# Kernel tuning notes

Measured on AMD Instinct MI355X. Metric: run time of the kernel, lower is better.

## Reference

```python
import jax, jax.numpy as jnp
import numpy as np

N = 100000
E = 1600000
DIN = 128
H = 4
C1 = 32   # hidden_dim per head, layer 1
C2 = 64   # output_dim, layer 2 (heads=1)
NEG_SLOPE = 0.2


def setup_inputs() -> dict:
    key = jax.random.key(0)
    ks = jax.random.split(key, 16)
    x = jax.random.normal(ks[0], (N, DIN), dtype=jnp.float32)
    src = jax.random.randint(ks[1], (E,), 0, N, dtype=jnp.int64)
    off = jax.random.randint(ks[2], (E,), 1, N, dtype=jnp.int64)
    dst = (src + off) % N  # guaranteed no self loops
    edge_index = jnp.stack([src, dst], axis=0)
    edge_weight = jax.random.uniform(ks[3], (E,), dtype=jnp.float32)
    g = 0.1
    # layer 1 params (heads=4, concat)
    W1 = jax.random.normal(ks[4], (DIN, H * C1), dtype=jnp.float32) * g
    att_src1 = jax.random.normal(ks[5], (H, C1), dtype=jnp.float32) * g
    att_dst1 = jax.random.normal(ks[6], (H, C1), dtype=jnp.float32) * g
    att_edge1 = jax.random.normal(ks[7], (H, C1), dtype=jnp.float32) * g
    We1 = jax.random.normal(ks[8], (1, H * C1), dtype=jnp.float32) * g
    b1 = jnp.zeros((H * C1,), dtype=jnp.float32)
    # layer 2 params (heads=1, no concat)
    W2 = jax.random.normal(ks[9], (H * C1, C2), dtype=jnp.float32) * g
    att_src2 = jax.random.normal(ks[10], (1, C2), dtype=jnp.float32) * g
    att_dst2 = jax.random.normal(ks[11], (1, C2), dtype=jnp.float32) * g
    att_edge2 = jax.random.normal(ks[12], (1, C2), dtype=jnp.float32) * g
    We2 = jax.random.normal(ks[13], (1, C2), dtype=jnp.float32) * g
    b2 = jnp.zeros((C2,), dtype=jnp.float32)
    return dict(x=x, edge_index=edge_index, edge_weight=edge_weight,
                W1=W1, att_src1=att_src1, att_dst1=att_dst1, att_edge1=att_edge1, We1=We1, b1=b1,
                W2=W2, att_src2=att_src2, att_dst2=att_dst2, att_edge2=att_edge2, We2=We2, b2=b2)


def gat_conv(x, src, dst, ew, W, a_src, a_dst, a_edge, We, b, heads, out_ch, concat):
    n = x.shape[0]
    xs = (x @ W).reshape(n, heads, out_ch)                 # [N,H,C]
    alpha_src = (xs * a_src[None]).sum(-1)                 # [N,H]
    alpha_dst = (xs * a_dst[None]).sum(-1)                 # [N,H]
    e = (ew[:, None] @ We).reshape(-1, heads, out_ch)      # [E,H,C]
    alpha_edge = (e * a_edge[None]).sum(-1)                # [E,H]
    alpha = alpha_src[src] + alpha_dst[dst] + alpha_edge   # [E,H]
    alpha = jax.nn.leaky_relu(alpha, NEG_SLOPE)
    # segment softmax over destination nodes (every node has a self loop)
    m = jax.ops.segment_max(alpha, dst, num_segments=n)
    ex = jnp.exp(alpha - m[dst])
    s = jax.ops.segment_sum(ex, dst, num_segments=n)
    att = ex / (s[dst] + 1e-16)                            # [E,H]
    out = jax.ops.segment_sum(xs[src] * att[:, :, None], dst, num_segments=n)  # [N,H,C]
    out = out.reshape(n, heads * out_ch) if concat else out.mean(axis=1)
    return out + b


def reference(x, edge_index, edge_weight,
              W1, att_src1, att_dst1, att_edge1, We1, b1,
              W2, att_src2, att_dst2, att_edge2, We2, b2):
    n = x.shape[0]
    src, dst = edge_index[0], edge_index[1]
    # add self loops with fill_value='mean' for edge weights (PyG default)
    si = jnp.arange(n, dtype=src.dtype)
    src2 = jnp.concatenate([src, si])
    dst2 = jnp.concatenate([dst, si])
    ew2 = jnp.concatenate([edge_weight, jnp.full((n,), edge_weight.mean(), dtype=edge_weight.dtype)])
    h = gat_conv(x, src2, dst2, ew2, W1, att_src1, att_dst1, att_edge1, We1, b1, H, C1, True)
    h = jax.nn.elu(h)
    # dropout is identity in eval mode
    out = gat_conv(h, src2, dst2, ew2, W2, att_src2, att_dst2, att_edge2, We2, b2, 1, C2, False)
    return out
```

## Files before the change

### kernel.cpp

```cpp
#include <hip/hip_runtime.h>
#include <hip/hip_fp16.h>
#include <math.h>

#define NN 100000
#define NE 1600000
#define DIN 128
#define NH 4
#define C1 32
#define C2 64
#define NEG 0.2f

#define SCAN_CHUNK 1024
#define NBLK ((NN + SCAN_CHUNK - 1) / SCAN_CHUNK)

#define NBUCK 8
#define BUCKN (NN / NBUCK)
#define CAPB 300000
#define BIN_CHUNK 4096
#define NBINBLK ((NE + BIN_CHUNK - 1) / BIN_CHUNK)

typedef __attribute__((ext_vector_type(8))) short bf16x8;
typedef __attribute__((ext_vector_type(4))) float f32x4;

__device__ __forceinline__ unsigned bf16rtn(float f) {
    unsigned b = __float_as_uint(f);
    return (b + 0x7FFFu + ((b >> 16) & 1u)) >> 16;
}
__device__ __forceinline__ unsigned pack2bf(float lo, float hi) {
    return bf16rtn(lo) | (bf16rtn(hi) << 16);
}
__device__ __forceinline__ unsigned pack2h(float lo, float hi) {
    unsigned a = __half_as_ushort(__float2half(lo));
    unsigned b = __half_as_ushort(__float2half(hi));
    return a | (b << 16);
}
__device__ __forceinline__ float h2f_bits(unsigned short u) {
    return __half2float(__ushort_as_half(u));
}

__global__ void k_setup(const float* __restrict__ We1, const float* __restrict__ ae1,
                        const float* __restrict__ We2, const float* __restrict__ ae2,
                        float* __restrict__ params) {
    __shared__ float sm[128];
    int t = threadIdx.x;
    sm[t] = We1[t] * ae1[t];
    __syncthreads();
    if (t < 4) {
        float s = 0.f;
        for (int c = 0; c < 32; c++) s += sm[t * 32 + c];
        params[2 + t] = s;
    }
    __syncthreads();
    if (t < 64) sm[t] = We2[t] * ae2[t];
    __syncthreads();
    if (t == 0) {
        float s = 0.f;
        for (int c = 0; c < 64; c++) s += sm[c];
        params[6] = s;
        params[1] = params[0] / (float)NE;
    }
}

__global__ void k_wprep(const float* __restrict__ W1, const float* __restrict__ W2,
                        uint4* __restrict__ wfrag1, uint4* __restrict__ wfrag2) {
    int t = blockIdx.x * 256 + threadIdx.x;
    if (t < 2048) {
        int f = t >> 6, l = t & 63;
        int n = f & 7, kc = f >> 3;
        int col = n * 16 + (l & 15);
        int kb = kc * 32 + (l >> 4) * 8;
        const float* p = W1 + (size_t)kb * 128 + col;
        uint4 pk;
        pk.x = pack2bf(p[0], p[128]);
        pk.y = pack2bf(p[256], p[384]);
        pk.z = pack2bf(p[512], p[640]);
        pk.w = pack2bf(p[768], p[896]);
        wfrag1[t] = pk;
    } else if (t < 3072) {
        int s = t - 2048;
        int f = s >> 6, l = s & 63;
        int n = f & 3, kc = f >> 2;
        int col = n * 16 + (l & 15);
        int kb = kc * 32 + (l >> 4) * 8;
        const float* p = W2 + (size_t)kb * 64 + col;
        uint4 pk;
        pk.x = pack2bf(p[0], p[64]);
        pk.y = pack2bf(p[128], p[192]);
        pk.z = pack2bf(p[256], p[320]);
        pk.w = pack2bf(p[384], p[448]);
        wfrag2[s] = pk;
    }
}

__global__ void k_binA(const int* __restrict__ srcI, const int* __restrict__ dstI,
                       const float* __restrict__ ew, int* __restrict__ bcur,
                       int* __restrict__ bdst, int2* __restrict__ bse,
                       float* __restrict__ params) {
    __shared__ int hcnt[NBUCK], hbase[NBUCK], hoff[NBUCK];
    int t = threadIdx.x;
    int e0 = blockIdx.x * BIN_CHUNK;
    if (t < NBUCK) hcnt[t] = 0;
    __syncthreads();
    for (int i = t; i < BIN_CHUNK; i += 256) {
        int e = e0 + i;
        if (e < NE) atomicAdd(&hcnt[dstI[e] / BUCKN], 1);
    }
    __syncthreads();
    if (t < NBUCK) { hbase[t] = atomicAdd(&bcur[t], hcnt[t]); hoff[t] = 0; }
    __syncthreads();
    float locw = 0.f;
    for (int i = t; i < BIN_CHUNK; i += 256) {
        int e = e0 + i;
        if (e < NE) {
            int d = dstI[e];
            float w = ew[e];
            locw += w;
            int b = d / BUCKN;
            int p = b * CAPB + hbase[b] + atomicAdd(&hoff[b], 1);
            bdst[p] = d;
            bse[p] = make_int2(srcI[e], __float_as_int(w));
        }
    }
    for (int o = 32; o > 0; o >>= 1) locw += __shfl_down(locw, o, 64);
    if ((t & 63) == 0) atomicAdd(&params[0], locw);
}

__global__ void k_histB(const int* __restrict__ bdst, const int* __restrict__ bcur,
                        int* __restrict__ deg) {
    int b = blockIdx.x & (NBUCK - 1);
    int slice = blockIdx.x >> 3;
    int cnt = bcur[b];
    int lo = b * CAPB;
    int per = (cnt + 255) / 256;
    int s0 = lo + slice * per;
    int s1 = min(s0 + per, lo + cnt);
    for (int i = s0 + threadIdx.x; i < s1; i += 256)
        atomicAdd(&deg[bdst[i]], 1);
}

__global__ void k_scanA(const int* __restrict__ deg, int* __restrict__ bsum) {
    __shared__ int ws[4];
    int b = blockIdx.x;
    int base = b * SCAN_CHUNK;
    int t = threadIdx.x;
    int s = 0;
    for (int i = t; i < SCAN_CHUNK; i += 256) {
        int idx = base + i;
        if (idx < NN) s += deg[idx];
    }
    for (int o = 32; o > 0; o >>= 1) s += __shfl_down(s, o, 64);
    int lane = t & 63, wid = t >> 6;
    if (lane == 0) ws[wid] = s;
    __syncthreads();
    if (t == 0) bsum[b] = ws[0] + ws[1] + ws[2] + ws[3];
}

__global__ void k_scanB(const int* __restrict__ bsum, int* __restrict__ bpre,
                        int* __restrict__ rowptr) {
    __shared__ int wtot[2];
    int t = threadIdx.x;
    int lane = t & 63, wid = t >> 6;
    int v = (t < NBLK) ? bsum[t] : 0;
    int inc = v;
    for (int o = 1; o < 64; o <<= 1) { int u = __shfl_up(inc, o, 64); if (lane >= o) inc += u; }
    if (lane == 63) wtot[wid] = inc;
    __syncthreads();
    if (wid == 1) inc += wtot[0];
    if (t < NBLK) bpre[t] = inc - v;
    if (t == NBLK - 1) rowptr[NN] = inc;
}

__global__ void k_scanC(const int* __restrict__ deg, const int* __restrict__ bpre,
                        int* __restrict__ rowptr, int* __restrict__ cursor) {
    __shared__ int wtot[4];
    int b = blockIdx.x;
    int t = threadIdx.x;
    int lane = t & 63, wid = t >> 6;
    int idx0 = b * SCAN_CHUNK + t * 4;
    int d[4];
    int s = 0;
    #pragma unroll
    for (int j = 0; j < 4; j++) {
        int idx = idx0 + j;
        d[j] = (idx < NN) ? deg[idx] : 0;
        s += d[j];
    }
    int inc = s;
    for (int o = 1; o < 64; o <<= 1) { int u = __shfl_up(inc, o, 64); if (lane >= o) inc += u; }
    if (lane == 63) wtot[wid] = inc;
    __syncthreads();
    int add = bpre[b];
    for (int w = 0; w < wid; w++) add += wtot[w];
    int excl = inc - s + add;
    #pragma unroll
    for (int j = 0; j < 4; j++) {
        int idx = idx0 + j;
        if (idx < NN) { rowptr[idx] = excl; cursor[idx] = excl; }
        excl += d[j];
    }
}

__global__ void k_binB(const int* __restrict__ bdst, const int2* __restrict__ bse,
                       const int* __restrict__ bcur, int* __restrict__ cursor,
                       const float* __restrict__ as1, const float* __restrict__ ad1,
                       const float* __restrict__ params, int4* __restrict__ edge4) {
    int b = blockIdx.x & (NBUCK - 1);
    int slice = blockIdx.x >> 3;
    int cnt = bcur[b];
    int lo = b * CAPB;
    int per = (cnt + 255) / 256;
    int s0 = lo + slice * per;
    int s1 = min(s0 + per, lo + cnt);
    float ce0 = params[2], ce1 = params[3], ce2 = params[4], ce3 = params[5];
    for (int i = s0 + threadIdx.x; i < s1; i += 256) {
        int d = bdst[i];
        int2 se = bse[i];
        float w = __int_as_float(se.y);
        float4 a1 = *(const float4*)(as1 + (size_t)se.x * 4);
        float4 d1 = *(const float4*)(ad1 + (size_t)d * 4);
        float q0 = a1.x + d1.x + w * ce0; q0 = q0 > 0.f ? q0 : NEG * q0;
        float q1 = a1.y + d1.y + w * ce1; q1 = q1 > 0.f ? q1 : NEG * q1;
        float q2 = a1.z + d1.z + w * ce2; q2 = q2 > 0.f ? q2 : NEG * q2;
        float q3 = a1.w + d1.w + w * ce3; q3 = q3 > 0.f ? q3 : NEG * q3;
        q0 = __expf(q0); q1 = __expf(q1); q2 = __expf(q2); q3 = __expf(q3);
        int idx = atomicAdd(&cursor[d], 1);
        edge4[idx] = make_int4(se.x, se.y, (int)pack2h(q0, q1), (int)pack2h(q2, q3));
    }
}


__global__ void __launch_bounds__(256, 4)
k_gemm1(const float* __restrict__ x, const uint4* __restrict__ wfrag1,
        const float* __restrict__ asv, const float* __restrict__ adv,
        unsigned* __restrict__ xs1b, float* __restrict__ as1, float* __restrict__ ad1) {
    __shared__ uint4 smem[2112];
    int t = threadIdx.x;
    for (int i = t; i < 2048; i += 256) smem[i] = wfrag1[i];
    __syncthreads();
    int wid = t >> 6, lane = t & 63;
    int r0 = blockIdx.x * 64 + wid * 16;
    int rowA = r0 + (lane & 15);
    int kb = (lane >> 4) * 8;
    bf16x8 afr[4];
    if (rowA < NN) {
        const float* xr = x + (size_t)rowA * 128 + kb;
        #pragma unroll
        for (int kc = 0; kc < 4; kc++) {
            float4 u0 = *(const float4*)(xr + kc * 32);
            float4 u1 = *(const float4*)(xr + kc * 32 + 4);
            uint4 p = make_uint4(pack2bf(u0.x, u0.y), pack2bf(u0.z, u0.w),
                                 pack2bf(u1.x, u1.y), pack2bf(u1.z, u1.w));
            afr[kc] = *(bf16x8*)&p;
        }
    } else {
        uint4 z = make_uint4(0u, 0u, 0u, 0u);
        #pragma unroll
        for (int kc = 0; kc < 4; kc++) afr[kc] = *(bf16x8*)&z;
    }
    f32x4 acc[8];
    #pragma unroll
    for (int n = 0; n < 8; n++) acc[n] = (f32x4){0.f, 0.f, 0.f, 0.f};
    #pragma unroll
    for (int kc = 0; kc < 4; kc++) {
        #pragma unroll
        for (int n = 0; n < 8; n++) {
            uint4 bw = smem[(kc * 8 + n) * 64 + lane];
            acc[n] = __builtin_amdgcn_mfma_f32_16x16x32_bf16(afr[kc], *(bf16x8*)&bw, acc[n], 0, 0, 0);
        }
    }
    __syncthreads();
    float* ef = (float*)smem + wid * 2112;
    #pragma unroll
    for (int n = 0; n < 8; n++) {
        #pragma unroll
        for (int r = 0; r < 4; r++) {
            int rw = (lane >> 4) * 4 + r;
            int col = n * 16 + (lane & 15);
            ef[rw * 132 + (col >> 5) * 33 + (col & 31)] = acc[n][r];
        }
    }
    __syncthreads();
    int rw = lane >> 2, head = lane & 3;
    int row = r0 + rw;
    if (row < NN) {
        const float* rb = ef + rw * 132 + head * 33;
        const float* av = asv + head * 32;
        const float* dv = adv + head * 32;
        unsigned* orow = xs1b + (size_t)row * 64 + head * 16;
        float ps = 0.f, pd = 0.f;
        #pragma unroll
        for (int j = 0; j < 4; j++) {
            float v[8];
            #pragma unroll
            for (int e = 0; e < 8; e++) {
                v[e] = rb[8 * j + e];
                ps += v[e] * av[8 * j + e];
                pd += v[e] * dv[8 * j + e];
            }
            uint4 pk = make_uint4(pack2bf(v[0], v[1]), pack2bf(v[2], v[3]),
                                  pack2bf(v[4], v[5]), pack2bf(v[6], v[7]));
            *(uint4*)(orow + 4 * j) = pk;
        }
        as1[row * 4 + head] = ps;
        ad1[row * 4 + head] = pd;
    }
}


__global__ void k_agg1(const unsigned* __restrict__ xs1b, const float* __restrict__ as1,
                       const float* __restrict__ ad1, const int* __restrict__ rowptr,
                       const int4* __restrict__ edge4,
                       const float* __restrict__ params, const float* __restrict__ b1,
                       unsigned* __restrict__ h1b) {
    int wid = threadIdx.x >> 6, lane = threadIdx.x & 63;
    int n = blockIdx.x * 4 + wid;
    if (n >= NN) return;
    int h = lane >> 4;
    float meanw = params[1];
    float aself = as1[n * 4 + h] + ad1[n * 4 + h] + meanw * params[2 + h];
    aself = aself > 0.f ? aself : NEG * aself;
    float qs = __expf(aself);
    unsigned us = xs1b[(size_t)n * 64 + lane];
    float s  = qs;
    float ax = qs * __uint_as_float(us << 16);
    float ay = qs * __uint_as_float(us & 0xFFFF0000u);
    int lo = rowptr[n], hi = rowptr[n + 1];
    int hlo = h < 2, hodd = h & 1;
    int i = lo;
    for (; i + 8 <= hi; i += 8) {
        int cj[8]; float qj[8]; unsigned vv[8];
        #pragma unroll
        for (int u = 0; u < 8; u++) {
            int4 er = edge4[i + u];
            cj[u] = er.x;
            unsigned qw = hlo ? (unsigned)er.z : (unsigned)er.w;
            qw = hodd ? (qw >> 16) : (qw & 0xFFFFu);
            qj[u] = h2f_bits((unsigned short)qw);
        }
        #pragma unroll
        for (int u = 0; u < 8; u++) vv[u] = xs1b[(size_t)cj[u] * 64 + lane];
        #pragma unroll
        for (int u = 0; u < 8; u++) {
            s += qj[u];
            ax += qj[u] * __uint_as_float(vv[u] << 16);
            ay += qj[u] * __uint_as_float(vv[u] & 0xFFFF0000u);
        }
    }
    for (; i < hi; i++) {
        int4 er = edge4[i];
        unsigned qw = hlo ? (unsigned)er.z : (unsigned)er.w;
        qw = hodd ? (qw >> 16) : (qw & 0xFFFFu);
        float qj = h2f_bits((unsigned short)qw);
        unsigned u = xs1b[(size_t)er.x * 64 + lane];
        s += qj;
        ax += qj * __uint_as_float(u << 16);
        ay += qj * __uint_as_float(u & 0xFFFF0000u);
    }
    float inv = 1.0f / (s + 1e-16f);
    float o0 = ax * inv + b1[2 * lane];
    float o1 = ay * inv + b1[2 * lane + 1];
    o0 = o0 > 0.f ? o0 : (__expf(o0) - 1.0f);
    o1 = o1 > 0.f ? o1 : (__expf(o1) - 1.0f);
    h1b[(size_t)n * 64 + lane] = pack2bf(o0, o1);
}


__global__ void __launch_bounds__(256, 6)
k_gemm2(const unsigned* __restrict__ h1b, const uint4* __restrict__ wfrag2,
        const float* __restrict__ asv, const float* __restrict__ adv,
        unsigned* __restrict__ xs2b, float* __restrict__ as2, float* __restrict__ ad2) {
    __shared__ uint4 smem[1056];
    int t = threadIdx.x;
    for (int i = t; i < 1024; i += 256) smem[i] = wfrag2[i];
    __syncthreads();
    int wid = t >> 6, lane = t & 63;
    int r0 = blockIdx.x * 64 + wid * 16;
    int rowA = r0 + (lane & 15);
    bf16x8 afr[4];
    if (rowA < NN) {
        const uint4* hr = (const uint4*)(h1b + (size_t)rowA * 64);
        #pragma unroll
        for (int kc = 0; kc < 4; kc++) {
            uint4 p = hr[kc * 4 + (lane >> 4)];
            afr[kc] = *(bf16x8*)&p;
        }
    } else {
        uint4 z = make_uint4(0u, 0u, 0u, 0u);
        #pragma unroll
        for (int kc = 0; kc < 4; kc++) afr[kc] = *(bf16x8*)&z;
    }
    f32x4 acc[4];
    #pragma unroll
    for (int n = 0; n < 4; n++) acc[n] = (f32x4){0.f, 0.f, 0.f, 0.f};
    #pragma unroll
    for (int kc = 0; kc < 4; kc++) {
        #pragma unroll
        for (int n = 0; n < 4; n++) {
            uint4 bw = smem[(kc * 4 + n) * 64 + lane];
            acc[n] = __builtin_amdgcn_mfma_f32_16x16x32_bf16(afr[kc], *(bf16x8*)&bw, acc[n], 0, 0, 0);
        }
    }
    __syncthreads();
    float* ef = (float*)smem + wid * 1056;
    #pragma unroll
    for (int n = 0; n < 4; n++) {
        #pragma unroll
        for (int r = 0; r < 4; r++) {
            int rw = (lane >> 4) * 4 + r;
            int col = n * 16 + (lane & 15);
            ef[rw * 66 + (col >> 5) * 33 + (col & 31)] = acc[n][r];
        }
    }
    __syncthreads();
    int rw = lane >> 2, q = lane & 3;
    int row = r0 + rw;
    const float* rb = ef + rw * 66 + (q >> 1) * 33 + (q & 1) * 16;
    const float* av = asv + q * 16;
    const float* dv = adv + q * 16;
    float ps = 0.f, pd = 0.f;
    unsigned pk[4];
    #pragma unroll
    for (int j = 0; j < 2; j++) {
        float v[8];
        #pragma unroll
        for (int e = 0; e < 8; e++) {
            v[e] = rb[8 * j + e];
            ps += v[e] * av[8 * j + e];
            pd += v[e] * dv[8 * j + e];
        }
        pk[0] = pack2bf(v[0], v[1]); pk[1] = pack2bf(v[2], v[3]);
        pk[2] = pack2bf(v[4], v[5]); pk[3] = pack2bf(v[6], v[7]);
        if (row < NN)
            *(uint4*)(xs2b + (size_t)row * 32 + q * 8 + 4 * j) = make_uint4(pk[0], pk[1], pk[2], pk[3]);
    }
    ps += __shfl_xor(ps, 1, 64); ps += __shfl_xor(ps, 2, 64);
    pd += __shfl_xor(pd, 1, 64); pd += __shfl_xor(pd, 2, 64);
    if (q == 0 && row < NN) { as2[row] = ps; ad2[row] = pd; }
}

__global__ void k_alpha2(int4* __restrict__ edge4, const float* __restrict__ as2,
                         const float* __restrict__ ad2, const int* __restrict__ rowptr,
                         const float* __restrict__ params) {
    int wid = threadIdx.x >> 6, lane = threadIdx.x & 63;
    int n = blockIdx.x * 4 + wid;
    if (n >= NN) return;
    float ce = params[6];
    float adn = ad2[n];
    int lo = rowptr[n], hi = rowptr[n + 1];
    for (int i = lo + lane; i < hi; i += 64) {
        int2 er = *(const int2*)&edge4[i];
        float a = as2[er.x] + adn + __int_as_float(er.y) * ce;
        a = a > 0.f ? a : NEG * a;
        ((int*)&edge4[i])[1] = __float_as_int(__expf(a));
    }
}


__global__ void k_agg2(const unsigned short* __restrict__ xs2h, const float* __restrict__ as2,
                       const float* __restrict__ ad2, const int* __restrict__ rowptr,
                       const int4* __restrict__ edge4,
                       const float* __restrict__ params, const float* __restrict__ b2,
                       float* __restrict__ out) {
    int wid = threadIdx.x >> 6, lane = threadIdx.x & 63;
    int n = blockIdx.x * 4 + wid;
    if (n >= NN) return;
    float ce = params[6];
    float meanw = params[1];
    float adn = ad2[n];
    float aself = as2[n] + adn + meanw * ce;
    aself = aself > 0.f ? aself : NEG * aself;
    float qs = __expf(aself);
    float s = qs;
    float ac = qs * __uint_as_float(((unsigned)xs2h[(size_t)n * 64 + lane]) << 16);
    int lo = rowptr[n], hi = rowptr[n + 1];
    int i = lo;
    for (; i + 8 <= hi; i += 8) {
        int cj[8]; float qj[8]; unsigned short vv[8];
        #pragma unroll
        for (int u = 0; u < 8; u++) {
            int2 er = *(const int2*)&edge4[i + u];
            cj[u] = er.x;
            qj[u] = __int_as_float(er.y);
        }
        #pragma unroll
        for (int u = 0; u < 8; u++) vv[u] = xs2h[(size_t)cj[u] * 64 + lane];
        #pragma unroll
        for (int u = 0; u < 8; u++) {
            s += qj[u];
            ac += qj[u] * __uint_as_float(((unsigned)vv[u]) << 16);
        }
    }
    for (; i < hi; i++) {
        int2 er = *(const int2*)&edge4[i];
        float qj = __int_as_float(er.y);
        float v = __uint_as_float(((unsigned)xs2h[(size_t)er.x * 64 + lane]) << 16);
        s += qj;
        ac += qj * v;
    }
    out[(size_t)n * 64 + lane] = ac / (s + 1e-16f) + b2[lane];
}

extern "C" void kernel_launch(void* const* d_in, const int* in_sizes, int n_in,
                              void* d_out, int out_size, void* d_ws, size_t ws_size,
                              hipStream_t stream) {
    const float* x    = (const float*)d_in[0];
    const int*   ei   = (const int*)d_in[1];
    const float* ew   = (const float*)d_in[2];
    const float* W1   = (const float*)d_in[3];
    const float* as1v = (const float*)d_in[4];
    const float* ad1v = (const float*)d_in[5];
    const float* ae1v = (const float*)d_in[6];
    const float* We1  = (const float*)d_in[7];
    const float* b1   = (const float*)d_in[8];
    const float* W2   = (const float*)d_in[9];
    const float* as2v = (const float*)d_in[10];
    const float* ad2v = (const float*)d_in[11];
    const float* ae2v = (const float*)d_in[12];
    const float* We2  = (const float*)d_in[13];
    const float* b2   = (const float*)d_in[14];
    const int* srcI = ei;
    const int* dstI = ei + NE;

    float* wsf = (float*)d_ws;
    size_t off = 0;
    auto alloc = [&](size_t nelts) { float* p = wsf + off; off += (nelts + 63) & ~(size_t)63; return p; };
    float*    params = alloc(64);
    int*      deg    = (int*)alloc(NN);
    int*      bcur   = (int*)alloc(64);
    int*      rowptr = (int*)alloc(NN + 1);
    int*      cursor = (int*)alloc(NN);
    int*      bsum   = (int*)alloc(NBLK);
    int*      bpre   = (int*)alloc(NBLK);
    uint4*    wfrag1 = (uint4*)alloc(8192);
    uint4*    wfrag2 = (uint4*)alloc(4096);
    size_t    binsOff = off;
    int*      bdst   = (int*)alloc((size_t)NBUCK * CAPB);
    int2*     bse    = (int2*)alloc((size_t)NBUCK * CAPB * 2);
    int4*     edge4  = (int4*)alloc((size_t)NE * 4);
    float*    as1    = alloc(NN * 4);
    float*    ad1    = alloc(NN * 4);
    unsigned* h1b    = (unsigned*)alloc((size_t)NN * 64);
    unsigned* xs1b   = (unsigned*)alloc((size_t)NN * 64);
    unsigned* xs2b   = (unsigned*)(wsf + binsOff);
    float*    as2 = as1;
    float*    ad2 = ad1;

    hipMemsetAsync(d_ws, 0, (64 + 100032 + 64) * sizeof(float), stream);

    k_wprep <<<12, 256, 0, stream>>>(W1, W2, wfrag1, wfrag2);
    k_binA  <<<NBINBLK, 256, 0, stream>>>(srcI, dstI, ew, bcur, bdst, bse, params);
    k_histB <<<2048, 256, 0, stream>>>(bdst, bcur, deg);
    k_scanA <<<NBLK, 256, 0, stream>>>(deg, bsum);
    k_scanB <<<1, 128, 0, stream>>>(bsum, bpre, rowptr);
    k_scanC <<<NBLK, 256, 0, stream>>>(deg, bpre, rowptr, cursor);
    k_setup <<<1, 128, 0, stream>>>(We1, ae1v, We2, ae2v, params);
    k_gemm1 <<<(NN + 63) / 64, 256, 0, stream>>>(x, wfrag1, as1v, ad1v, xs1b, as1, ad1);
    k_binB  <<<2048, 256, 0, stream>>>(bdst, bse, bcur, cursor, as1, ad1, params, edge4);
    k_agg1  <<<25000, 256, 0, stream>>>(xs1b, as1, ad1, rowptr, edge4, params, b1, h1b);
    k_gemm2 <<<(NN + 63) / 64, 256, 0, stream>>>(h1b, wfrag2, as2v, ad2v, xs2b, as2, ad2);
    k_alpha2<<<25000, 256, 0, stream>>>(edge4, as2, ad2, rowptr, params);
    k_agg2  <<<25000, 256, 0, stream>>>((const unsigned short*)xs2b, as2, ad2, rowptr, edge4, params, b2, (float*)d_out);
}
```

Measured before the change: 423.1 us.

## Fuse layer-2 attention into aggregation and load edges cooperatively via shuffles

Removes the separate k_alpha2 kernel and computes the layer-2 edge attention exponentials inside k_agg2. Each lane loads one edge record and the values are broadcast with wave shuffles. In k_agg1, edge records are likewise loaded once per lane group (16 edges per wave iteration) and broadcast by shuffle, so every lane no longer redundantly reads the full int4 for every edge. This saves a kernel launch, one read-modify-write pass over edge4, and redundant edge loads, at the cost of extra shuffle instructions and larger unrolled register arrays.

After: 403.6 us. -4.6%, faster.

```diff
diff --git a/kernel.cpp b/kernel.cpp
--- a/kernel.cpp
+++ b/kernel.cpp
@@ -316,6 +316,7 @@
     int n = blockIdx.x * 4 + wid;
     if (n >= NN) return;
     int h = lane >> 4;
+    int h4 = lane & 3;
     float meanw = params[1];
     float aself = as1[n * 4 + h] + ad1[n * 4 + h] + meanw * params[2 + h];
     aself = aself > 0.f ? aself : NEG * aself;
@@ -325,36 +326,44 @@
     float ax = qs * __uint_as_float(us << 16);
     float ay = qs * __uint_as_float(us & 0xFFFF0000u);
     int lo = rowptr[n], hi = rowptr[n + 1];
-    int hlo = h < 2, hodd = h & 1;
-    int i = lo;
-    for (; i + 8 <= hi; i += 8) {
-        int cj[8]; float qj[8]; unsigned vv[8];
-        #pragma unroll
-        for (int u = 0; u < 8; u++) {
-            int4 er = edge4[i + u];
-            cj[u] = er.x;
-            unsigned qw = hlo ? (unsigned)er.z : (unsigned)er.w;
-            qw = hodd ? (qw >> 16) : (qw & 0xFFFFu);
-            qj[u] = h2f_bits((unsigned short)qw);
-        }
-        #pragma unroll
-        for (int u = 0; u < 8; u++) vv[u] = xs1b[(size_t)cj[u] * 64 + lane];
-        #pragma unroll
-        for (int u = 0; u < 8; u++) {
-            s += qj[u];
-            ax += qj[u] * __uint_as_float(vv[u] << 16);
-            ay += qj[u] * __uint_as_float(vv[u] & 0xFFFF0000u);
-        }
-    }
-    for (; i < hi; i++) {
-        int4 er = edge4[i];
-        unsigned qw = hlo ? (unsigned)er.z : (unsigned)er.w;
-        qw = hodd ? (qw >> 16) : (qw & 0xFFFFu);
-        float qj = h2f_bits((unsigned short)qw);
-        unsigned u = xs1b[(size_t)er.x * 64 + lane];
-        s += qj;
-        ax += qj * __uint_as_float(u << 16);
-        ay += qj * __uint_as_float(u & 0xFFFF0000u);
+    for (int base = lo; base < hi; base += 16) {
+        int e = lane >> 2;
+        int idx = base + e;
+        int cx = 0;
+        float q = 0.f;
+        if (idx < hi) {
+            int4 er = edge4[idx];
+            cx = er.x;
+            unsigned qw = (h4 < 2) ? (unsigned)er.z : (unsigned)er.w;
+            qw = (h4 & 1) ? (qw >> 16) : (qw & 0xFFFFu);
+            q = h2f_bits((unsigned short)qw);
+        }
+        int m = hi - base; if (m > 16) m = 16;
+        if (m == 16) {
+            int cj[16]; float qj[16]; unsigned vv[16];
+            #pragma unroll
+            for (int j = 0; j < 16; j++) {
+                cj[j] = __shfl(cx, 4 * j, 64);
+                qj[j] = __shfl(q, 4 * j + h, 64);
+            }
+            #pragma unroll
+            for (int j = 0; j < 16; j++) vv[j] = xs1b[(size_t)cj[j] * 64 + lane];
+            #pragma unroll
+            for (int j = 0; j < 16; j++) {
+                s += qj[j];
+                ax += qj[j] * __uint_as_float(vv[j] << 16);
+                ay += qj[j] * __uint_as_float(vv[j] & 0xFFFF0000u);
+            }
+        } else {
+            for (int j = 0; j < m; j++) {
+                int cj = __shfl(cx, 4 * j, 64);
+                float qj = __shfl(q, 4 * j + h, 64);
+                unsigned u = xs1b[(size_t)cj * 64 + lane];
+                s += qj;
+                ax += qj * __uint_as_float(u << 16);
+                ay += qj * __uint_as_float(u & 0xFFFF0000u);
+            }
+        }
     }
     float inv = 1.0f / (s + 1e-16f);
     float o0 = ax * inv + b1[2 * lane];
@@ -436,23 +445,6 @@
     ps += __shfl_xor(ps, 1, 64); ps += __shfl_xor(ps, 2, 64);
     pd += __shfl_xor(pd, 1, 64); pd += __shfl_xor(pd, 2, 64);
     if (q == 0 && row < NN) { as2[row] = ps; ad2[row] = pd; }
-}
-
-__global__ void k_alpha2(int4* __restrict__ edge4, const float* __restrict__ as2,
-                         const float* __restrict__ ad2, const int* __restrict__ rowptr,
-                         const float* __restrict__ params) {
-    int wid = threadIdx.x >> 6, lane = threadIdx.x & 63;
-    int n = blockIdx.x * 4 + wid;
-    if (n >= NN) return;
-    float ce = params[6];
-    float adn = ad2[n];
-    int lo = rowptr[n], hi = rowptr[n + 1];
-    for (int i = lo + lane; i < hi; i += 64) {
-        int2 er = *(const int2*)&edge4[i];
-        float a = as2[er.x] + adn + __int_as_float(er.y) * ce;
-        a = a > 0.f ? a : NEG * a;
-        ((int*)&edge4[i])[1] = __float_as_int(__expf(a));
-    }
 }
 
 
@@ -473,29 +465,40 @@
     float s = qs;
     float ac = qs * __uint_as_float(((unsigned)xs2h[(size_t)n * 64 + lane]) << 16);
     int lo = rowptr[n], hi = rowptr[n + 1];
-    int i = lo;
-    for (; i + 8 <= hi; i += 8) {
-        int cj[8]; float qj[8]; unsigned short vv[8];
-        #pragma unroll
-        for (int u = 0; u < 8; u++) {
-            int2 er = *(const int2*)&edge4[i + u];
-            cj[u] = er.x;
-            qj[u] = __int_as_float(er.y);
-        }
-        #pragma unroll
-        for (int u = 0; u < 8; u++) vv[u] = xs2h[(size_t)cj[u] * 64 + lane];
-        #pragma unroll
-        for (int u = 0; u < 8; u++) {
-            s += qj[u];
-            ac += qj[u] * __uint_as_float(((unsigned)vv[u]) << 16);
-        }
-    }
-    for (; i < hi; i++) {
-        int2 er = *(const int2*)&edge4[i];
-        float qj = __int_as_float(er.y);
-        float v = __uint_as_float(((unsigned)xs2h[(size_t)er.x * 64 + lane]) << 16);
-        s += qj;
-        ac += qj * v;
+    for (int base = lo; base < hi; base += 64) {
+        int idx = base + lane;
+        int cx = 0;
+        float q = 0.f;
+        if (idx < hi) {
+            int2 er = *(const int2*)&edge4[idx];
+            cx = er.x;
+            float a = as2[cx] + adn + __int_as_float(er.y) * ce;
+            a = a > 0.f ? a : NEG * a;
+            q = __expf(a);
+        }
+        int m = hi - base; if (m > 64) m = 64;
+        int j = 0;
+        for (; j + 16 <= m; j += 16) {
+            int cj[16]; float qj[16]; unsigned short vv[16];
+            #pragma unroll
+            for (int u = 0; u < 16; u++) {
+                cj[u] = __shfl(cx, j + u, 64);
+                qj[u] = __shfl(q, j + u, 64);
+            }
+            #pragma unroll
+            for (int u = 0; u < 16; u++) vv[u] = xs2h[(size_t)cj[u] * 64 + lane];
+            #pragma unroll
+            for (int u = 0; u < 16; u++) {
+                s += qj[u];
+                ac += qj[u] * __uint_as_float(((unsigned)vv[u]) << 16);
+            }
+        }
+        for (; j < m; j++) {
+            int cj = __shfl(cx, j, 64);
+            float qj = __shfl(q, j, 64);
+            s += qj;
+            ac += qj * __uint_as_float(((unsigned)xs2h[(size_t)cj * 64 + lane]) << 16);
+        }
     }
     out[(size_t)n * 64 + lane] = ac / (s + 1e-16f) + b2[lane];
 }
@@ -558,6 +561,5 @@
     k_binB  <<<2048, 256, 0, stream>>>(bdst, bse, bcur, cursor, as1, ad1, params, edge4);
     k_agg1  <<<25000, 256, 0, stream>>>(xs1b, as1, ad1, rowptr, edge4, params, b1, h1b);
     k_gemm2 <<<(NN + 63) / 64, 256, 0, stream>>>(h1b, wfrag2, as2v, ad2v, xs2b, as2, ad2);
-    k_alpha2<<<25000, 256, 0, stream>>>(edge4, as2, ad2, rowptr, params);
     k_agg2  <<<25000, 256, 0, stream>>>((const unsigned short*)xs2b, as2, ad2, rowptr, edge4, params, b2, (float*)d_out);
 }
```
